# Kernel tuning notes

Measured on AMD Instinct MI355X. Metric: run time of the kernel, lower is better.

The kernel has to match this reference:

```python
import jax, jax.numpy as jnp
import numpy as np

N_NODES = 100000  # size_u + size_v + size_w
N_MP = 3          # metapaths vv, uu, ww
N_EDGES = 1000000
D_IN = 64
D_OUT = 64


def setup_inputs() -> dict:
    key = jax.random.key(0)
    k1, k2, k3, k4 = jax.random.split(key, 4)
    x = jax.random.normal(k1, (N_NODES, D_IN), dtype=jnp.float32)
    # per-metapath GCNConv weight (glorot-ish scale)
    W = jax.random.normal(k2, (N_MP, D_IN, D_OUT), dtype=jnp.float32) * (1.0 / np.sqrt(D_IN))
    edge_index = jax.random.randint(k3, (N_MP, 2, N_EDGES), 0, N_NODES, dtype=jnp.int64)
    edge_weight = jax.random.uniform(k4, (N_MP, N_EDGES), dtype=jnp.float32)
    return {"x": x, "W": W, "edge_index": edge_index, "edge_weight": edge_weight}


def _gcn_conv(x, w_mat, row, col, ew, num_nodes):
    # gcn_norm without self-loops: deg[i] = sum of edge weights into i
    deg = jax.ops.segment_sum(ew, col, num_segments=num_nodes)
    dinv = jnp.where(deg > 0, jax.lax.rsqrt(jnp.where(deg > 0, deg, 1.0)), 0.0)
    norm = dinv[row] * ew * dinv[col]          # [E]
    h = x @ w_mat                               # [N, D_OUT]
    msg = h[row] * norm[:, None]                # [E, D_OUT] gather + scale
    return jax.ops.segment_sum(msg, col, num_segments=num_nodes)  # scatter-add


def reference(x, W, edge_index, edge_weight):
    num_nodes = x.shape[0]
    outs = []
    for i in range(N_MP):  # small fixed loop over structurally distinct encoders
        row = edge_index[i, 0]
        col = edge_index[i, 1]
        out = _gcn_conv(x, W[i], row, col, edge_weight[i], num_nodes)
        outs.append(jax.nn.relu(out))  # act=nn.ReLU
    return jnp.stack(outs)  # [3, N, D_OUT]; dropout omitted (eval mode)
```

## Files before the change

### kernel.cpp

```cpp
#include <hip/hip_runtime.h>

#define NNODES 100000
#define NMP 3
#define NEDGES 1000000
#define D 64
#define NTOT (NMP * NNODES)
#define BINW 1024
#define NBIN 293
#define CAPB 10944
#define T1 3072
#define OVCAP 131072

typedef __attribute__((ext_vector_type(8))) short bf16x8;
typedef __attribute__((ext_vector_type(4))) float floatx4;

__device__ __forceinline__ unsigned short f2bf(float f) {
    unsigned u = __float_as_uint(f);
    u = (u + 0x7FFFu + ((u >> 16) & 1u)) >> 16;
    return (unsigned short)u;
}
__device__ __forceinline__ float bf2f_lo(unsigned u) { return __uint_as_float(u << 16); }
__device__ __forceinline__ float bf2f_hi(unsigned u) { return __uint_as_float(u & 0xFFFF0000u); }

__global__ __launch_bounds__(512) void split_kernel(const int* __restrict__ ei,
                                                    const float* __restrict__ ew,
                                                    int* __restrict__ gcur,
                                                    int* __restrict__ ovcur,
                                                    int* __restrict__ ovf,
                                                    uint2* __restrict__ A) {
    __shared__ int hist[NBIN], cur[NBIN];
    const int t = threadIdx.x;
    const int mp = blockIdx.y;
    const int e0 = blockIdx.x * T1;
    for (int i = t; i < NBIN; i += 512) hist[i] = 0;
    __syncthreads();
    unsigned key[6]; float w[6]; int bn[6];
#pragma unroll
    for (int i = 0; i < 6; ++i) {
        int e = e0 + i * 512 + t;
        bn[i] = -1;
        if (e < NEDGES) {
            int r = ei[(mp * 2 + 0) * NEDGES + e];
            int c = ei[(mp * 2 + 1) * NEDGES + e];
            w[i] = ew[mp * NEDGES + e];
            int cflat = mp * NNODES + c;
            int rflat = mp * NNODES + r;
            int b = cflat >> 10;
            bn[i] = b;
            key[i] = ((unsigned)(cflat & 1023) << 19) | (unsigned)rflat;
            atomicAdd(&hist[b], 1);
        }
    }
    __syncthreads();
    for (int i = t; i < NBIN; i += 512) {
        int v = hist[i];
        cur[i] = v ? atomicAdd(&gcur[i], v) : 0;
    }
    __syncthreads();
#pragma unroll
    for (int i = 0; i < 6; ++i) {
        if (bn[i] >= 0) {
            int pos = atomicAdd(&cur[bn[i]], 1);
            if (pos < CAPB) {
                A[(size_t)bn[i] * CAPB + pos] = make_uint2(key[i], __float_as_uint(w[i]));
            } else {
                int op = atomicAdd(ovcur, 1);
                if (op < OVCAP) {
                    int cflat = (bn[i] << 10) | (int)(key[i] >> 19);
                    ovf[3 * op] = cflat;
                    ovf[3 * op + 1] = (int)(key[i] & 0x7FFFFu);
                    ovf[3 * op + 2] = __float_as_int(w[i]);
                }
            }
        }
    }
}

__global__ __launch_bounds__(256) void compact2_kernel(const int* __restrict__ gcur,
                                                       const uint2* __restrict__ A,
                                                       const int* __restrict__ ovcur,
                                                       const int* __restrict__ ovf,
                                                       uint2* __restrict__ C,
                                                       int2* __restrict__ nodeoff,
                                                       float* __restrict__ dinv) {
    const int bin = blockIdx.x;
    __shared__ int cnt[BINW];
    __shared__ float wsum[BINW];
    __shared__ int pos[BINW];
    __shared__ int sh[256];
    const int t = threadIdx.x;
    for (int i = t; i < BINW; i += 256) { cnt[i] = 0; wsum[i] = 0.0f; }
    __syncthreads();
    const int len = min(gcur[bin], CAPB);
    const uint2* Ab = A + (size_t)bin * CAPB;
    for (int p = t; p < len; p += 256) {
        uint2 rec = Ab[p];
        atomicAdd(&cnt[rec.x >> 19], 1);
        atomicAdd(&wsum[rec.x >> 19], __uint_as_float(rec.y));
    }
    const int ovn = min(*ovcur, OVCAP);
    for (int i = t; i < ovn; i += 256) {
        int cflat = ovf[3 * i];
        if ((cflat >> 10) == bin) {
            atomicAdd(&cnt[cflat & 1023], 1);
            atomicAdd(&wsum[cflat & 1023], __int_as_float(ovf[3 * i + 2]));
        }
    }
    __syncthreads();
    int c0 = cnt[4 * t], c1 = cnt[4 * t + 1], c2 = cnt[4 * t + 2], c3 = cnt[4 * t + 3];
    int vsum = c0 + c1 + c2 + c3;
    sh[t] = vsum;
    __syncthreads();
    for (int d = 1; d < 256; d <<= 1) {
        int add = (t >= d) ? sh[t - d] : 0;
        __syncthreads();
        sh[t] += add;
        __syncthreads();
    }
    const int base = bin * CAPB;
    const int lim = base + CAPB;
    int p0 = base + sh[t] - vsum;
    int p1 = p0 + c0, p2 = p1 + c1, p3 = p2 + c2;
    pos[4 * t] = p0; pos[4 * t + 1] = p1; pos[4 * t + 2] = p2; pos[4 * t + 3] = p3;
    int starts[4] = {p0, p1, p2, p3};
    int cs[4] = {c0, c1, c2, c3};
#pragma unroll
    for (int j = 0; j < 4; ++j) {
        int cl = 4 * t + j;
        int node = (bin << 10) + cl;
        if (node < NTOT) {
            nodeoff[node] = make_int2(starts[j], cs[j]);
            float dg = wsum[cl];
            dinv[node] = (dg > 0.0f) ? rsqrtf(dg) : 0.0f;
        }
    }
    __syncthreads();
    for (int p = t; p < len; p += 256) {
        uint2 rec = Ab[p];
        int s = atomicAdd(&pos[rec.x >> 19], 1);
        if (s < lim) C[s] = make_uint2(rec.x & 0x7FFFFu, rec.y);
    }
    for (int i = t; i < ovn; i += 256) {
        int cflat = ovf[3 * i];
        if ((cflat >> 10) == bin) {
            int s = atomicAdd(&pos[cflat & 1023], 1);
            if (s < lim) C[s] = make_uint2((unsigned)ovf[3 * i + 1], (unsigned)ovf[3 * i + 2]);
        }
    }
}

__global__ __launch_bounds__(256) void prep_w_kernel(const float* __restrict__ W,
                                                     unsigned short* __restrict__ wT) {
    int idx = blockIdx.x * 256 + threadIdx.x;
    if (idx >= NMP * D * D) return;
    int mp = idx >> 12, rem = idx & 4095;
    int k = rem >> 6, n = rem & 63;
    wT[(mp * D + n) * D + k] = f2bf(W[idx]);
}

__global__ __launch_bounds__(256) void gemm_kernel(const float* __restrict__ x,
                                                   const unsigned short* __restrict__ wT,
                                                   const float* __restrict__ dinv,
                                                   unsigned short* __restrict__ h) {
    const int wave = threadIdx.x >> 6;
    const int lane = threadIdx.x & 63;
    const int rowbase = (blockIdx.x * 4 + wave) * 16;
    if (rowbase >= NNODES) return;
    const int m = lane & 15;
    const int q = lane >> 4;
    const float4* xr = (const float4*)(x + (size_t)(rowbase + m) * D);
    bf16x8 a[2];
#pragma unroll
    for (int kc = 0; kc < 2; ++kc) {
        float4 x0 = xr[kc * 8 + q * 2];
        float4 x1 = xr[kc * 8 + q * 2 + 1];
        a[kc][0] = f2bf(x0.x); a[kc][1] = f2bf(x0.y);
        a[kc][2] = f2bf(x0.z); a[kc][3] = f2bf(x0.w);
        a[kc][4] = f2bf(x1.x); a[kc][5] = f2bf(x1.y);
        a[kc][6] = f2bf(x1.z); a[kc][7] = f2bf(x1.w);
    }
#pragma unroll
    for (int mp = 0; mp < NMP; ++mp) {
        float dv = dinv[mp * NNODES + rowbase + m];
#pragma unroll
        for (int nt = 0; nt < 4; ++nt) {
            const bf16x8* bp = (const bf16x8*)(wT + (size_t)(mp * D + nt * 16 + m) * D);
            bf16x8 b0 = bp[q];
            bf16x8 b1 = bp[4 + q];
            floatx4 acc = {0.f, 0.f, 0.f, 0.f};
            acc = __builtin_amdgcn_mfma_f32_16x16x32_bf16(b0, a[0], acc, 0, 0, 0);
            acc = __builtin_amdgcn_mfma_f32_16x16x32_bf16(b1, a[1], acc, 0, 0, 0);
            unsigned v0 = (unsigned)f2bf(acc[0] * dv) | ((unsigned)f2bf(acc[1] * dv) << 16);
            unsigned v1 = (unsigned)f2bf(acc[2] * dv) | ((unsigned)f2bf(acc[3] * dv) << 16);
            *(uint2*)(h + ((size_t)mp * NNODES + rowbase + m) * D + nt * 16 + q * 4) =
                make_uint2(v0, v1);
        }
    }
}

__global__ __launch_bounds__(256) void gather_kernel(const int2* __restrict__ nodeoff,
                                                     const uint2* __restrict__ dense,
                                                     const unsigned short* __restrict__ h,
                                                     const float* __restrict__ dinv,
                                                     float* __restrict__ out) {
    const int tid = threadIdx.x;
    const int wave = tid >> 6, lane = tid & 63;
    const int sub = lane >> 5;
    const int g = (lane >> 3) & 3;
    const int f = lane & 7;
    const int w = blockIdx.x * 8 + wave * 2 + sub;
    int2 off = nodeoff[w];
    const int start = off.x, end = off.x + off.y;
    const uint4* hp = (const uint4*)h;
    float acc[8] = {0, 0, 0, 0, 0, 0, 0, 0};
    if (end > start) {
        const int last = end - 1;
        uint2 prA = dense[min(start + g, last)];
        uint2 prB = dense[min(start + 4 + g, last)];
        uint4 hvA = hp[(size_t)prA.x * 8 + f];
        for (int p = start; p < end; p += 4) {
            uint2 prC = dense[min(p + 8 + g, last)];
            uint4 hvB = hp[(size_t)prB.x * 8 + f];
            float wgt = (p + g < end) ? __uint_as_float(prA.y) : 0.0f;
            acc[0] += wgt * bf2f_lo(hvA.x); acc[1] += wgt * bf2f_hi(hvA.x);
            acc[2] += wgt * bf2f_lo(hvA.y); acc[3] += wgt * bf2f_hi(hvA.y);
            acc[4] += wgt * bf2f_lo(hvA.z); acc[5] += wgt * bf2f_hi(hvA.z);
            acc[6] += wgt * bf2f_lo(hvA.w); acc[7] += wgt * bf2f_hi(hvA.w);
            prA = prB; hvA = hvB; prB = prC;
        }
    }
#pragma unroll
    for (int j = 0; j < 8; ++j) {
        acc[j] += __shfl_xor(acc[j], 8);
        acc[j] += __shfl_xor(acc[j], 16);
    }
    float dv = dinv[w];
    if (g < 2) {
        float4 o = g ? make_float4(acc[4], acc[5], acc[6], acc[7])
                     : make_float4(acc[0], acc[1], acc[2], acc[3]);
        o.x = fmaxf(o.x * dv, 0.0f);
        o.y = fmaxf(o.y * dv, 0.0f);
        o.z = fmaxf(o.z * dv, 0.0f);
        o.w = fmaxf(o.w * dv, 0.0f);
        ((float4*)out)[(size_t)w * 16 + f * 2 + g] = o;
    }
}

extern "C" void kernel_launch(void* const* d_in, const int* in_sizes, int n_in,
                              void* d_out, int out_size, void* d_ws, size_t ws_size,
                              hipStream_t stream) {
    const float* x  = (const float*)d_in[0];
    const float* W  = (const float*)d_in[1];
    const int*   ei = (const int*)d_in[2];
    const float* ew = (const float*)d_in[3];
    float* out = (float*)d_out;

    char* ws = (char*)d_ws;
    uint2* A           = (uint2*)(ws + 0);
    unsigned short* h  = (unsigned short*)(ws + 0);
    uint2* C           = (uint2*)(ws + 38400000);
    int2*  nodeoff     = (int2*)(ws + 64052736);
    float* dinv        = (float*)(ws + 66452736);
    unsigned short* wT = (unsigned short*)(ws + 67652736);
    int*   gcur        = (int*)(ws + 67677312);
    int*   ovcur       = (int*)(ws + 67678484);
    int*   ovf         = (int*)(ws + 67678488);

    hipMemsetAsync(gcur, 0, 1176, stream);

    split_kernel<<<dim3((NEDGES + T1 - 1) / T1, NMP), 512, 0, stream>>>(ei, ew, gcur,
                                                                        ovcur, ovf, A);
    compact2_kernel<<<NBIN, 256, 0, stream>>>(gcur, A, ovcur, ovf, C, nodeoff, dinv);
    prep_w_kernel<<<(NMP * D * D + 255) / 256, 256, 0, stream>>>(W, wT);
    gemm_kernel<<<(NNODES / 16 + 3) / 4, 256, 0, stream>>>(x, wT, dinv, h);
    gather_kernel<<<NTOT / 8, 256, 0, stream>>>(nodeoff, C, h, dinv, out);
}
```

Before: 286.9 us.

## Aggregate raw bf16 features first, then apply per-metapath GEMM with fused ReLU

Reorders the GCN computation to aggregate over neighbours first and transform afterwards. It gathers from a single shared bf16 copy of x, which is 12.8 MB instead of the three per-metapath h arrays totalling 38.4 MB, so the gather working set is a third of the size and more cache-friendly. Source-side dinv is now loaded per edge inside the gather. The aggregate is stored in bf16 and a new GEMM kernel applies W and ReLU to produce the output. This adds an extra bf16 round-trip of the aggregate, an extra prep kernel, and an additional per-edge dinv load.

After: 317.8 us. 1.11x slower.

```diff
diff --git a/kernel.cpp b/kernel.cpp
--- a/kernel.cpp
+++ b/kernel.cpp
@@ -149,6 +149,19 @@
     }
 }
 
+__global__ __launch_bounds__(256) void prep_x_kernel(const float* __restrict__ x,
+                                                     unsigned short* __restrict__ xb) {
+    int idx = blockIdx.x * 256 + threadIdx.x;
+    if (idx >= NNODES * D / 8) return;
+    const float4* xp = (const float4*)x;
+    float4 v0 = xp[idx * 2], v1 = xp[idx * 2 + 1];
+    unsigned u0 = (unsigned)f2bf(v0.x) | ((unsigned)f2bf(v0.y) << 16);
+    unsigned u1 = (unsigned)f2bf(v0.z) | ((unsigned)f2bf(v0.w) << 16);
+    unsigned u2 = (unsigned)f2bf(v1.x) | ((unsigned)f2bf(v1.y) << 16);
+    unsigned u3 = (unsigned)f2bf(v1.z) | ((unsigned)f2bf(v1.w) << 16);
+    ((uint4*)xb)[idx] = make_uint4(u0, u1, u2, u3);
+}
+
 __global__ __launch_bounds__(256) void prep_w_kernel(const float* __restrict__ W,
                                                      unsigned short* __restrict__ wT) {
     int idx = blockIdx.x * 256 + threadIdx.x;
@@ -158,75 +171,38 @@
     wT[(mp * D + n) * D + k] = f2bf(W[idx]);
 }
 
-__global__ __launch_bounds__(256) void gemm_kernel(const float* __restrict__ x,
-                                                   const unsigned short* __restrict__ wT,
-                                                   const float* __restrict__ dinv,
-                                                   unsigned short* __restrict__ h) {
-    const int wave = threadIdx.x >> 6;
-    const int lane = threadIdx.x & 63;
-    const int rowbase = (blockIdx.x * 4 + wave) * 16;
-    if (rowbase >= NNODES) return;
-    const int m = lane & 15;
-    const int q = lane >> 4;
-    const float4* xr = (const float4*)(x + (size_t)(rowbase + m) * D);
-    bf16x8 a[2];
-#pragma unroll
-    for (int kc = 0; kc < 2; ++kc) {
-        float4 x0 = xr[kc * 8 + q * 2];
-        float4 x1 = xr[kc * 8 + q * 2 + 1];
-        a[kc][0] = f2bf(x0.x); a[kc][1] = f2bf(x0.y);
-        a[kc][2] = f2bf(x0.z); a[kc][3] = f2bf(x0.w);
-        a[kc][4] = f2bf(x1.x); a[kc][5] = f2bf(x1.y);
-        a[kc][6] = f2bf(x1.z); a[kc][7] = f2bf(x1.w);
-    }
-#pragma unroll
-    for (int mp = 0; mp < NMP; ++mp) {
-        float dv = dinv[mp * NNODES + rowbase + m];
-#pragma unroll
-        for (int nt = 0; nt < 4; ++nt) {
-            const bf16x8* bp = (const bf16x8*)(wT + (size_t)(mp * D + nt * 16 + m) * D);
-            bf16x8 b0 = bp[q];
-            bf16x8 b1 = bp[4 + q];
-            floatx4 acc = {0.f, 0.f, 0.f, 0.f};
-            acc = __builtin_amdgcn_mfma_f32_16x16x32_bf16(b0, a[0], acc, 0, 0, 0);
-            acc = __builtin_amdgcn_mfma_f32_16x16x32_bf16(b1, a[1], acc, 0, 0, 0);
-            unsigned v0 = (unsigned)f2bf(acc[0] * dv) | ((unsigned)f2bf(acc[1] * dv) << 16);
-            unsigned v1 = (unsigned)f2bf(acc[2] * dv) | ((unsigned)f2bf(acc[3] * dv) << 16);
-            *(uint2*)(h + ((size_t)mp * NNODES + rowbase + m) * D + nt * 16 + q * 4) =
-                make_uint2(v0, v1);
-        }
-    }
-}
-
 __global__ __launch_bounds__(256) void gather_kernel(const int2* __restrict__ nodeoff,
                                                      const uint2* __restrict__ dense,
-                                                     const unsigned short* __restrict__ h,
+                                                     const unsigned short* __restrict__ xb,
                                                      const float* __restrict__ dinv,
-                                                     float* __restrict__ out) {
+                                                     unsigned short* __restrict__ agg) {
     const int tid = threadIdx.x;
     const int wave = tid >> 6, lane = tid & 63;
     const int sub = lane >> 5;
     const int g = (lane >> 3) & 3;
     const int f = lane & 7;
     const int w = blockIdx.x * 8 + wave * 2 + sub;
+    const int base = (w / NNODES) * NNODES;
     int2 off = nodeoff[w];
     const int start = off.x, end = off.x + off.y;
-    const uint4* hp = (const uint4*)h;
+    const uint4* xp = (const uint4*)xb;
     float acc[8] = {0, 0, 0, 0, 0, 0, 0, 0};
     if (end > start) {
         const int last = end - 1;
         uint2 prA = dense[min(start + g, last)];
         uint2 prB = dense[min(start + 4 + g, last)];
-        uint4 hvA = hp[(size_t)prA.x * 8 + f];
+        uint4 hvA = xp[(size_t)(prA.x - base) * 8 + f];
+        float dvA = dinv[prA.x];
         for (int p = start; p < end; p += 4) {
             uint2 prC = dense[min(p + 8 + g, last)];
-            uint4 hvB = hp[(size_t)prB.x * 8 + f];
-            float wgt = (p + g < end) ? __uint_as_float(prA.y) : 0.0f;
+            uint4 hvB = xp[(size_t)(prB.x - base) * 8 + f];
+            float dvB = dinv[prB.x];
+            float wgt = (p + g < end) ? __uint_as_float(prA.y) * dvA : 0.0f;
             acc[0] += wgt * bf2f_lo(hvA.x); acc[1] += wgt * bf2f_hi(hvA.x);
             acc[2] += wgt * bf2f_lo(hvA.y); acc[3] += wgt * bf2f_hi(hvA.y);
             acc[4] += wgt * bf2f_lo(hvA.z); acc[5] += wgt * bf2f_hi(hvA.z);
             acc[6] += wgt * bf2f_lo(hvA.w); acc[7] += wgt * bf2f_hi(hvA.w);
-            prA = prB; hvA = hvB; prB = prC;
+            prA = prB; hvA = hvB; dvA = dvB; prB = prC;
         }
     }
 #pragma unroll
@@ -234,15 +210,40 @@
         acc[j] += __shfl_xor(acc[j], 8);
         acc[j] += __shfl_xor(acc[j], 16);
     }
-    float dv = dinv[w];
-    if (g < 2) {
-        float4 o = g ? make_float4(acc[4], acc[5], acc[6], acc[7])
-                     : make_float4(acc[0], acc[1], acc[2], acc[3]);
-        o.x = fmaxf(o.x * dv, 0.0f);
-        o.y = fmaxf(o.y * dv, 0.0f);
-        o.z = fmaxf(o.z * dv, 0.0f);
-        o.w = fmaxf(o.w * dv, 0.0f);
-        ((float4*)out)[(size_t)w * 16 + f * 2 + g] = o;
+    if (g == 0) {
+        float dv = dinv[w];
+        unsigned u0 = (unsigned)f2bf(acc[0] * dv) | ((unsigned)f2bf(acc[1] * dv) << 16);
+        unsigned u1 = (unsigned)f2bf(acc[2] * dv) | ((unsigned)f2bf(acc[3] * dv) << 16);
+        unsigned u2 = (unsigned)f2bf(acc[4] * dv) | ((unsigned)f2bf(acc[5] * dv) << 16);
+        unsigned u3 = (unsigned)f2bf(acc[6] * dv) | ((unsigned)f2bf(acc[7] * dv) << 16);
+        ((uint4*)agg)[(size_t)w * 8 + f] = make_uint4(u0, u1, u2, u3);
+    }
+}
+
+__global__ __launch_bounds__(256) void gemm2_kernel(const unsigned short* __restrict__ agg,
+                                                    const unsigned short* __restrict__ wT,
+                                                    float* __restrict__ out) {
+    const int wave = threadIdx.x >> 6;
+    const int lane = threadIdx.x & 63;
+    const int rowbase = (blockIdx.x * 4 + wave) * 16;
+    if (rowbase >= NTOT) return;
+    const int mp = rowbase / NNODES;
+    const int m = lane & 15;
+    const int q = lane >> 4;
+    const bf16x8* ar = (const bf16x8*)(agg + (size_t)(rowbase + m) * D);
+    bf16x8 a0 = ar[q];
+    bf16x8 a1 = ar[4 + q];
+#pragma unroll
+    for (int nt = 0; nt < 4; ++nt) {
+        const bf16x8* bp = (const bf16x8*)(wT + (size_t)(mp * D + nt * 16 + m) * D);
+        bf16x8 b0 = bp[q];
+        bf16x8 b1 = bp[4 + q];
+        floatx4 acc = {0.f, 0.f, 0.f, 0.f};
+        acc = __builtin_amdgcn_mfma_f32_16x16x32_bf16(b0, a0, acc, 0, 0, 0);
+        acc = __builtin_amdgcn_mfma_f32_16x16x32_bf16(b1, a1, acc, 0, 0, 0);
+        float4 o = make_float4(fmaxf(acc[0], 0.0f), fmaxf(acc[1], 0.0f),
+                               fmaxf(acc[2], 0.0f), fmaxf(acc[3], 0.0f));
+        *(float4*)(out + (size_t)(rowbase + m) * D + nt * 16 + q * 4) = o;
     }
 }
 
@@ -257,7 +258,7 @@
 
     char* ws = (char*)d_ws;
     uint2* A           = (uint2*)(ws + 0);
-    unsigned short* h  = (unsigned short*)(ws + 0);
+    unsigned short* agg= (unsigned short*)(ws + 0);
     uint2* C           = (uint2*)(ws + 38400000);
     int2*  nodeoff     = (int2*)(ws + 64052736);
     float* dinv        = (float*)(ws + 66452736);
@@ -265,13 +266,15 @@
     int*   gcur        = (int*)(ws + 67677312);
     int*   ovcur       = (int*)(ws + 67678484);
     int*   ovf         = (int*)(ws + 67678488);
+    unsigned short* xb = (unsigned short*)(ws + 69251352);
 
     hipMemsetAsync(gcur, 0, 1176, stream);
 
     split_kernel<<<dim3((NEDGES + T1 - 1) / T1, NMP), 512, 0, stream>>>(ei, ew, gcur,
                                                                         ovcur, ovf, A);
     compact2_kernel<<<NBIN, 256, 0, stream>>>(gcur, A, ovcur, ovf, C, nodeoff, dinv);
+    prep_x_kernel<<<(NNODES * D / 8 + 255) / 256, 256, 0, stream>>>(x, xb);
     prep_w_kernel<<<(NMP * D * D + 255) / 256, 256, 0, stream>>>(W, wT);
-    gemm_kernel<<<(NNODES / 16 + 3) / 4, 256, 0, stream>>>(x, wT, dinv, h);
-    gather_kernel<<<NTOT / 8, 256, 0, stream>>>(nodeoff, C, h, dinv, out);
-}
+    gather_kernel<<<NTOT / 8, 256, 0, stream>>>(nodeoff, C, xb, dinv, agg);
+    gemm2_kernel<<<(NTOT / 16 + 3) / 4, 256, 0, stream>>>(agg, wT, out);
+}
```
